# Kernel optimization log

Hardware: AMD Instinct MI355X
Metric: run time of the kernel (lower is better)

## Reference

```python
import jax, jax.numpy as jnp
import numpy as np

N = 100_000   # nodes
E = 3_200_000  # edges (avg degree 32)


def setup_inputs() -> dict:
    key = jax.random.key(0)
    ks = jax.random.split(key, 8)
    x = jax.random.normal(ks[0], (N, 4), dtype=jnp.float32)
    edge_index = jax.random.randint(ks[1], (2, E), 0, N, dtype=jnp.int64)
    # GCNConv weights: lin(in,out,bias=False) then bias added post-aggregation
    W1 = jax.random.normal(ks[2], (4, 16), dtype=jnp.float32) * 0.5
    b1 = jax.random.normal(ks[3], (16,), dtype=jnp.float32) * 0.1
    W2 = jax.random.normal(ks[4], (16, 32), dtype=jnp.float32) * 0.25
    b2 = jax.random.normal(ks[5], (32,), dtype=jnp.float32) * 0.1
    Wfc = jax.random.normal(ks[6], (32, 4), dtype=jnp.float32) * 0.2
    bfc = jax.random.normal(ks[7], (4,), dtype=jnp.float32) * 0.1
    return {"x": x, "edge_index": edge_index, "W1": W1, "b1": b1,
            "W2": W2, "b2": b2, "Wfc": Wfc, "bfc": bfc}


def _gcn_conv(x, W, b, src, dst, norm):
    # h_j = x_j @ W ; out_i = sum_{j->i} norm_ij * h_j ; + bias
    n = x.shape[0]
    h = x @ W
    msg = h[src] * norm[:, None]              # [E+N, out]
    out = jax.ops.segment_sum(msg, dst, num_segments=n)
    return out + b


def reference(x, edge_index, W1, b1, W2, b2, Wfc, bfc):
    n = x.shape[0]
    loops = jnp.arange(n, dtype=edge_index.dtype)
    src = jnp.concatenate([edge_index[0], loops])  # PyG: row = source j
    dst = jnp.concatenate([edge_index[1], loops])  # col = target i
    # symmetric normalization with self-loops (PyG gcn_norm default)
    deg = jax.ops.segment_sum(jnp.ones(dst.shape[0], x.dtype), dst, num_segments=n)
    dinv = jnp.where(deg > 0, jax.lax.rsqrt(deg), jnp.zeros_like(deg))
    norm = dinv[src] * dinv[dst]

    h = jax.nn.relu(_gcn_conv(x, W1, b1, src, dst, norm))
    h = jax.nn.relu(_gcn_conv(h, W2, b2, src, dst, norm))
    return h @ Wfc + bfc
```

## Files before the change

kernel.cpp:

```cpp
#include <hip/hip_runtime.h>
#include <hip/hip_bf16.h>
#include <hip/hip_fp16.h>


#define NBUCK 1024
#define TILE  4096
#define EPT   8
#define BSH   7
#define CAP   5120

__global__ __launch_bounds__(512)
void k_bucket(const int* __restrict__ src, const int* __restrict__ dst,
              int* __restrict__ gcur, int* __restrict__ colbkt, int E) {
    __shared__ int hist[NBUCK];
    __shared__ int cur[NBUCK];
    __shared__ int scanW[8];
    __shared__ int reorder[TILE];
    int t = threadIdx.x;
    int tb = blockIdx.x * TILE;
    int cntT = min(TILE, E - tb);

    hist[t] = 0; hist[t + 512] = 0;
    __syncthreads();

    int sv[EPT], dv[EPT];
    #pragma unroll
    for (int j = 0; j < EPT; j++) {
        int i = t + j * 512;
        bool ok = i < cntT;
        sv[j] = ok ? src[tb + i] : 0;
        dv[j] = ok ? dst[tb + i] : 0;
        if (ok) atomicAdd(&hist[dv[j] >> BSH], 1);
    }
    __syncthreads();

    int b0 = t * 2;
    int h0 = hist[b0], h1 = hist[b0 + 1];
    int s = h0 + h1;
    int lane = t & 63, wid = t >> 6;
    int incl = s;
    #pragma unroll
    for (int off = 1; off < 64; off <<= 1) {
        int v = __shfl_up(incl, off);
        if (lane >= off) incl += v;
    }
    if (lane == 63) scanW[wid] = incl;
    __syncthreads();
    int wbase = 0;
    #pragma unroll
    for (int wI = 0; wI < 8; wI++) wbase += (wI < wid) ? scanW[wI] : 0;
    int ex = wbase + incl - s;
    cur[b0] = ex;
    cur[b0 + 1] = ex + h0;
    __syncthreads();

    #pragma unroll
    for (int j = 0; j < EPT; j++) {
        int i = t + j * 512;
        if (i < cntT) {
            int b = dv[j] >> BSH;
            int r = atomicAdd(&cur[b], 1);
            reorder[r] = sv[j] | ((dv[j] & ((1 << BSH) - 1)) << 17);
        }
    }
    __syncthreads();

    #pragma unroll
    for (int j = 0; j < 2; j++) {
        int b = b0 + j;
        int c = hist[b];
        if (c > 0) {
            int gb = atomicAdd(&gcur[b], c);
            int lo = cur[b] - c;
            for (int k = 0; k < c; k++) {
                int idx = gb + k;
                if (idx < CAP) colbkt[(size_t)b * CAP + idx] = reorder[lo + k];
            }
        }
    }
}

__global__ __launch_bounds__(256)
void k_sortpre(const int* __restrict__ gcur, int* __restrict__ colbkt,
               const float* __restrict__ x, float* __restrict__ dinv,
               __half* __restrict__ g1h, int* __restrict__ rowbeg,
               int* __restrict__ rowlen, int n) {
    __shared__ int recbuf[CAP];
    __shared__ int sorted[CAP];
    __shared__ int hist[128];
    __shared__ int offs[128];
    __shared__ int cur[128];
    __shared__ int wtot;
    int t = threadIdx.x, b = blockIdx.x;
    int nb = min(gcur[b], CAP);
    int* row = colbkt + (size_t)b * CAP;
    if (t < 128) hist[t] = 0;
    __syncthreads();
    for (int e = t; e < nb; e += 256) {
        int rec = __builtin_nontemporal_load(row + e);
        recbuf[e] = rec;
        atomicAdd(&hist[(rec >> 17) & 127], 1);
    }
    __syncthreads();
    int h = (t < 128) ? hist[t] : 0;
    int lane = t & 63;
    int incl = h;
    #pragma unroll
    for (int off = 1; off < 64; off <<= 1) {
        int v = __shfl_up(incl, off);
        if (lane >= off) incl += v;
    }
    if (t == 63) wtot = incl;
    __syncthreads();
    if (t < 128) {
        int incl2 = incl + ((t >= 64) ? wtot : 0);
        offs[t] = incl2;
        cur[t] = incl2 - h;
    }
    __syncthreads();
    for (int e = t; e < nb; e += 256) {
        int rec = recbuf[e];
        int dl = (rec >> 17) & 127;
        int p = atomicAdd(&cur[dl], 1);
        sorted[p] = rec;
    }
    __syncthreads();
    for (int e = t; e < nb; e += 256)
        __builtin_nontemporal_store(sorted[e], row + e);
    if (t < 128) {
        int node = (b << BSH) + t;
        if (node < n) {
            int len = hist[t];
            rowlen[node] = len;
            rowbeg[node] = b * CAP + (offs[t] - len);
            float di = rsqrtf((float)len + 1.0f);
            dinv[node] = di;
            float4 xv = *reinterpret_cast<const float4*>(x + (size_t)node * 4);
            union { __half2 h2[2]; uint2 u2; } pk;
            pk.h2[0] = __floats2half2_rn(di * xv.x, di * xv.y);
            pk.h2[1] = __floats2half2_rn(di * xv.z, di * xv.w);
            *reinterpret_cast<uint2*>(g1h + (size_t)node * 4) = pk.u2;
        }
    }
}

__device__ __forceinline__ void add_g1(float& a0, float& a1, float& a2, float& a3,
                                       uint2 u) {
    float2 f0 = __half22float2(*reinterpret_cast<const __half2*>(&u.x));
    float2 f1 = __half22float2(*reinterpret_cast<const __half2*>(&u.y));
    a0 += f0.x; a1 += f0.y; a2 += f1.x; a3 += f1.y;
}

__global__ __launch_bounds__(256)
void k_gather1(const int* __restrict__ rowbeg, const int* __restrict__ rowlen,
               const int* __restrict__ colbkt, const __half* __restrict__ g1h,
               const float* __restrict__ dinv, const float* __restrict__ W1,
               const float* __restrict__ b1, __half* __restrict__ g2h, int n) {
    __shared__ float w[64];
    __shared__ float bb[16];
    if (threadIdx.x < 64) w[threadIdx.x] = W1[threadIdx.x];
    if (threadIdx.x >= 64 && threadIdx.x < 80) bb[threadIdx.x - 64] = b1[threadIdx.x - 64];
    __syncthreads();
    int gt = blockIdx.x * 256 + threadIdx.x;
    int i = gt >> 2;
    int lane = gt & 3;
    if (i >= n) return;
    int len = rowlen[i];
    const int* row = colbkt + rowbeg[i];
    const uint2* g1v = reinterpret_cast<const uint2*>(g1h);
    float a0 = 0.f, a1 = 0.f, a2 = 0.f, a3 = 0.f;
    if (lane == 0)
        add_g1(a0, a1, a2, a3, g1v[i]);
    int e = lane;
    for (; e + 12 < len; e += 16) {
        int r0 = __builtin_nontemporal_load(row + e);
        int r1 = __builtin_nontemporal_load(row + e + 4);
        int r2 = __builtin_nontemporal_load(row + e + 8);
        int r3 = __builtin_nontemporal_load(row + e + 12);
        uint2 u0 = g1v[r0 & 0x1FFFF];
        uint2 u1 = g1v[r1 & 0x1FFFF];
        uint2 u2 = g1v[r2 & 0x1FFFF];
        uint2 u3 = g1v[r3 & 0x1FFFF];
        add_g1(a0, a1, a2, a3, u0);
        add_g1(a0, a1, a2, a3, u1);
        add_g1(a0, a1, a2, a3, u2);
        add_g1(a0, a1, a2, a3, u3);
    }
    for (; e < len; e += 4) {
        int rec = __builtin_nontemporal_load(row + e);
        add_g1(a0, a1, a2, a3, g1v[rec & 0x1FFFF]);
    }
    a0 += __shfl_xor(a0, 1); a1 += __shfl_xor(a1, 1);
    a2 += __shfl_xor(a2, 1); a3 += __shfl_xor(a3, 1);
    a0 += __shfl_xor(a0, 2); a1 += __shfl_xor(a1, 2);
    a2 += __shfl_xor(a2, 2); a3 += __shfl_xor(a3, 2);
    if (lane != 0) return;
    float di = dinv[i];
    a0 *= di; a1 *= di; a2 *= di; a3 *= di;
    union { __half2 h2[8]; uint4 u4[2]; } pk;
    #pragma unroll
    for (int c = 0; c < 8; c++) {
        int f0 = 2 * c, f1 = 2 * c + 1;
        float r0 = di * fmaxf(a0*w[f0] + a1*w[16+f0] + a2*w[32+f0] + a3*w[48+f0] + bb[f0], 0.f);
        float r1 = di * fmaxf(a0*w[f1] + a1*w[16+f1] + a2*w[32+f1] + a3*w[48+f1] + bb[f1], 0.f);
        pk.h2[c] = __floats2half2_rn(r0, r1);
    }
    uint4* o = reinterpret_cast<uint4*>(g2h + (size_t)i * 16);
    o[0] = pk.u4[0];
    o[1] = pk.u4[1];
}

__device__ __forceinline__ void add_g2(float* acc, uint4 a, uint4 b) {
    const __half2* pa = reinterpret_cast<const __half2*>(&a);
    const __half2* pb = reinterpret_cast<const __half2*>(&b);
    #pragma unroll
    for (int j = 0; j < 4; j++) {
        float2 f = __half22float2(pa[j]);
        acc[2*j] += f.x; acc[2*j+1] += f.y;
    }
    #pragma unroll
    for (int j = 0; j < 4; j++) {
        float2 f = __half22float2(pb[j]);
        acc[8+2*j] += f.x; acc[8+2*j+1] += f.y;
    }
}

__global__ __launch_bounds__(256)
void k_gather2(const int* __restrict__ rowbeg, const int* __restrict__ rowlen,
               const int* __restrict__ colbkt, const __half* __restrict__ g2h,
               const float* __restrict__ dinv, const float* __restrict__ W2,
               const float* __restrict__ b2, const float* __restrict__ Wfc,
               const float* __restrict__ bfc, float* __restrict__ out, int n) {
    __shared__ float w2[512];
    __shared__ float wf[128];
    __shared__ float b2s[32];
    __shared__ float bfs[4];
    for (int j = threadIdx.x; j < 512; j += blockDim.x) w2[j] = W2[j];
    if (threadIdx.x < 128) wf[threadIdx.x] = Wfc[threadIdx.x];
    if (threadIdx.x >= 128 && threadIdx.x < 160) b2s[threadIdx.x - 128] = b2[threadIdx.x - 128];
    if (threadIdx.x >= 160 && threadIdx.x < 164) bfs[threadIdx.x - 160] = bfc[threadIdx.x - 160];
    __syncthreads();

    int gt = blockIdx.x * 256 + threadIdx.x;
    int i = gt >> 3;
    int lane = gt & 7;
    if (i >= n) return;
    int len = rowlen[i];
    const int* row = colbkt + rowbeg[i];
    const uint4* g2v = reinterpret_cast<const uint4*>(g2h);

    float acc[16];
    #pragma unroll
    for (int k = 0; k < 16; k++) acc[k] = 0.f;
    if (lane == 0)
        add_g2(acc, g2v[(size_t)i * 2], g2v[(size_t)i * 2 + 1]);
    int e = lane;
    for (; e + 24 < len; e += 32) {
        int r0 = __builtin_nontemporal_load(row + e);
        int r1 = __builtin_nontemporal_load(row + e + 8);
        int r2 = __builtin_nontemporal_load(row + e + 16);
        int r3 = __builtin_nontemporal_load(row + e + 24);
        size_t s0 = (size_t)(r0 & 0x1FFFF) * 2;
        size_t s1 = (size_t)(r1 & 0x1FFFF) * 2;
        size_t s2 = (size_t)(r2 & 0x1FFFF) * 2;
        size_t s3 = (size_t)(r3 & 0x1FFFF) * 2;
        uint4 a0 = g2v[s0], c0 = g2v[s0 + 1];
        uint4 a1 = g2v[s1], c1 = g2v[s1 + 1];
        uint4 a2 = g2v[s2], c2 = g2v[s2 + 1];
        uint4 a3 = g2v[s3], c3 = g2v[s3 + 1];
        add_g2(acc, a0, c0);
        add_g2(acc, a1, c1);
        add_g2(acc, a2, c2);
        add_g2(acc, a3, c3);
    }
    for (; e < len; e += 8) {
        int rec = __builtin_nontemporal_load(row + e);
        size_t s = (size_t)(rec & 0x1FFFF) * 2;
        add_g2(acc, g2v[s], g2v[s + 1]);
    }
    #pragma unroll
    for (int k = 0; k < 16; k++) acc[k] += __shfl_xor(acc[k], 1);
    #pragma unroll
    for (int k = 0; k < 16; k++) acc[k] += __shfl_xor(acc[k], 2);
    #pragma unroll
    for (int k = 0; k < 16; k++) acc[k] += __shfl_xor(acc[k], 4);

    float di = dinv[i];
    #pragma unroll
    for (int k = 0; k < 16; k++) acc[k] *= di;

    float o0 = (lane == 0) ? bfs[0] : 0.f;
    float o1 = (lane == 0) ? bfs[1] : 0.f;
    float o2 = (lane == 0) ? bfs[2] : 0.f;
    float o3 = (lane == 0) ? bfs[3] : 0.f;
    int fbase = lane * 4;
    #pragma unroll
    for (int fo = 0; fo < 4; fo++) {
        int f = fbase + fo;
        float h = b2s[f];
        #pragma unroll
        for (int k = 0; k < 16; k++) h += acc[k] * w2[k * 32 + f];
        h = fmaxf(h, 0.0f);
        o0 += h * wf[f * 4 + 0];
        o1 += h * wf[f * 4 + 1];
        o2 += h * wf[f * 4 + 2];
        o3 += h * wf[f * 4 + 3];
    }
    o0 += __shfl_xor(o0, 1); o1 += __shfl_xor(o1, 1);
    o2 += __shfl_xor(o2, 1); o3 += __shfl_xor(o3, 1);
    o0 += __shfl_xor(o0, 2); o1 += __shfl_xor(o1, 2);
    o2 += __shfl_xor(o2, 2); o3 += __shfl_xor(o3, 2);
    o0 += __shfl_xor(o0, 4); o1 += __shfl_xor(o1, 4);
    o2 += __shfl_xor(o2, 4); o3 += __shfl_xor(o3, 4);
    if (lane != 0) return;
    float4 r; r.x = o0; r.y = o1; r.z = o2; r.w = o3;
    *reinterpret_cast<float4*>(out + (size_t)i * 4) = r;
}

extern "C" void kernel_launch(void* const* d_in, const int* in_sizes, int n_in,
                              void* d_out, int out_size, void* d_ws, size_t ws_size,
                              hipStream_t stream) {
    const float* x   = (const float*)d_in[0];
    const int*   ei  = (const int*)d_in[1];
    const float* W1  = (const float*)d_in[2];
    const float* b1  = (const float*)d_in[3];
    const float* W2  = (const float*)d_in[4];
    const float* b2  = (const float*)d_in[5];
    const float* Wfc = (const float*)d_in[6];
    const float* bfc = (const float*)d_in[7];
    float* out = (float*)d_out;

    const int n = in_sizes[0] / 4;
    const int E = in_sizes[1] / 2;
    const int* src = ei;
    const int* dst = ei + E;

    char* p = (char*)d_ws;
    int*    gcur   = (int*)p;           p += (size_t)NBUCK * 4;
    int*    colbkt = (int*)p;           p += (size_t)NBUCK * CAP * 4;
    int*    rowbeg = (int*)p;           p += (size_t)n * 4;
    int*    rowlen = (int*)p;           p += (size_t)n * 4;
    float*  dinv   = (float*)p;         p += (size_t)n * 4;
    __half* g1h    = (__half*)p;        p += (size_t)n * 8;
    __half* g2h    = (__half*)p;        p += (size_t)n * 32;

    const int NBu = (n + 127) >> BSH;
    const int gT  = (E + TILE - 1) / TILE;
    const int gN4 = ((size_t)n * 4 + 255) / 256;
    const int gN8 = ((size_t)n * 8 + 255) / 256;

    hipMemsetAsync(gcur, 0, (size_t)NBUCK * sizeof(int), stream);

    k_bucket <<<gT,  512, 0, stream>>>(src, dst, gcur, colbkt, E);
    k_sortpre<<<NBu, 256, 0, stream>>>(gcur, colbkt, x, dinv, g1h, rowbeg, rowlen, n);
    k_gather1<<<gN4, 256, 0, stream>>>(rowbeg, rowlen, colbkt, g1h, dinv, W1, b1, g2h, n);
    k_gather2<<<gN8, 256, 0, stream>>>(rowbeg, rowlen, colbkt, g2h, dinv,
                                       W2, b2, Wfc, bfc, out, n);
}
```

Before: 139.8 us.

## Scatter edges directly to global buckets, dropping the LDS reorder stage

The bucketing kernel no longer scans the histogram and stages edges in a shared-memory reorder buffer. Each bucket now reserves its global slot range with one atomic per block up front, and every edge is then written straight to colbkt at a position taken from a per-bucket shared atomic counter. The tile also grows to 6144 edges, with 12 per thread. This removes a scan, two barriers and the serial per-bucket copy loop. The cost is that global writes become scattered rather than contiguous runs, which may coalesce worse.

```diff
diff --git a/kernel.cpp b/kernel.cpp
--- a/kernel.cpp
+++ b/kernel.cpp
@@ -4,8 +4,8 @@
 
 
 #define NBUCK 1024
-#define TILE  4096
-#define EPT   8
+#define TILE  6144
+#define EPT   12
 #define BSH   7
 #define CAP   5120
 
@@ -13,9 +13,7 @@
 void k_bucket(const int* __restrict__ src, const int* __restrict__ dst,
               int* __restrict__ gcur, int* __restrict__ colbkt, int E) {
     __shared__ int hist[NBUCK];
-    __shared__ int cur[NBUCK];
-    __shared__ int scanW[8];
-    __shared__ int reorder[TILE];
+    __shared__ int wcur[NBUCK];
     int t = threadIdx.x;
     int tb = blockIdx.x * TILE;
     int cntT = min(TILE, E - tb);
@@ -34,24 +32,12 @@
     }
     __syncthreads();
 
-    int b0 = t * 2;
-    int h0 = hist[b0], h1 = hist[b0 + 1];
-    int s = h0 + h1;
-    int lane = t & 63, wid = t >> 6;
-    int incl = s;
-    #pragma unroll
-    for (int off = 1; off < 64; off <<= 1) {
-        int v = __shfl_up(incl, off);
-        if (lane >= off) incl += v;
-    }
-    if (lane == 63) scanW[wid] = incl;
-    __syncthreads();
-    int wbase = 0;
-    #pragma unroll
-    for (int wI = 0; wI < 8; wI++) wbase += (wI < wid) ? scanW[wI] : 0;
-    int ex = wbase + incl - s;
-    cur[b0] = ex;
-    cur[b0 + 1] = ex + h0;
+    #pragma unroll
+    for (int j = 0; j < NBUCK / 512; j++) {
+        int b = t + j * 512;
+        int c = hist[b];
+        wcur[b] = (c > 0) ? atomicAdd(&gcur[b], c) : 0;
+    }
     __syncthreads();
 
     #pragma unroll
@@ -59,23 +45,10 @@
         int i = t + j * 512;
         if (i < cntT) {
             int b = dv[j] >> BSH;
-            int r = atomicAdd(&cur[b], 1);
-            reorder[r] = sv[j] | ((dv[j] & ((1 << BSH) - 1)) << 17);
-        }
-    }
-    __syncthreads();
-
-    #pragma unroll
-    for (int j = 0; j < 2; j++) {
-        int b = b0 + j;
-        int c = hist[b];
-        if (c > 0) {
-            int gb = atomicAdd(&gcur[b], c);
-            int lo = cur[b] - c;
-            for (int k = 0; k < c; k++) {
-                int idx = gb + k;
-                if (idx < CAP) colbkt[(size_t)b * CAP + idx] = reorder[lo + k];
-            }
+            int pos = atomicAdd(&wcur[b], 1);
+            if (pos < CAP)
+                colbkt[(size_t)b * CAP + pos] =
+                    sv[j] | ((dv[j] & ((1 << BSH) - 1)) << 17);
         }
     }
 }
```

Result: faster. 126.8 us (-9.3%).
